# Optimization experiments

Hardware: AMD Instinct MI355X
Metric: run time of the kernel (lower is better)

The kernel has to match this reference:

```python
import jax, jax.numpy as jnp
import numpy as np

IMG_X, IMG_Y = 1333.0, 402.0   # image_size
MIN_SIZE = 16.0
NMS_THRESH = 0.7
PRE = 12000                    # n_train_pre_nms
POST = 2000                    # n_train_post_nms
HH, WW, A = 83, 25, 9          # 1333//16, 402//16, anchors per cell
N_ANCH = HH * WW * A           # 18675
B = 16


def setup_inputs() -> dict:
    key = jax.random.key(0)
    k1, k2, k3, k4, k5, k6 = jax.random.split(key, 6)
    # realistic anchor boxes inside the image
    xc = jax.random.uniform(k1, (N_ANCH,)) * IMG_X
    yc = jax.random.uniform(k2, (N_ANCH,)) * IMG_Y
    bw = jax.random.uniform(k3, (N_ANCH,)) * 240.0 + 16.0
    bh = jax.random.uniform(k4, (N_ANCH,)) * 120.0 + 16.0
    anchor_boxes = jnp.stack([xc - 0.5 * bw, yc - 0.5 * bh, xc + 0.5 * bw, yc + 0.5 * bh], axis=1)
    rpn_cls_score = jax.random.normal(k5, (B, N_ANCH * 2), dtype=jnp.float32)
    rpn_bbox_pred = jax.random.normal(k6, (B, N_ANCH, 4), dtype=jnp.float32) * 0.2
    return dict(anchor_boxes=anchor_boxes, rpn_cls_score=rpn_cls_score,
                rpn_bbox_pred=rpn_bbox_pred, rpn_cls_loss=jnp.zeros((1,), jnp.float32),
                rpn_bbox_loss=jnp.zeros((1,), jnp.float32))


def _decode(anchor_boxes, rpn_bbox_pred):
    ah = anchor_boxes[:, 3] - anchor_boxes[:, 1]
    aw = anchor_boxes[:, 2] - anchor_boxes[:, 0]
    acy = anchor_boxes[:, 1] + 0.5 * ah
    acx = anchor_boxes[:, 0] + 0.5 * aw
    dx = rpn_bbox_pred[..., 0]
    dy = rpn_bbox_pred[..., 1]
    dw = rpn_bbox_pred[..., 2]
    dh = rpn_bbox_pred[..., 3]
    cy = dy * ah + acy
    cx = dx * aw + acx
    h = jnp.exp(dh) * ah
    w = jnp.exp(dw) * aw
    # clip: x coords to [0, image_size[0]], y coords to [0, image_size[1]] (as in source)
    x1 = jnp.clip(cx - 0.5 * w, 0.0, IMG_X)
    y1 = jnp.clip(cy - 0.5 * h, 0.0, IMG_Y)
    x2 = jnp.clip(cx + 0.5 * w, 0.0, IMG_X)
    y2 = jnp.clip(cy + 0.5 * h, 0.0, IMG_Y)
    return jnp.stack([x1, y1, x2, y2], axis=-1)  # [N,4] broadcast over batch -> [B,N,4]


def _nms_one(roi, score):
    # roi: [N,4], score: [N]
    hs = roi[:, 3] - roi[:, 1]
    ws = roi[:, 2] - roi[:, 0]
    valid = (hs >= MIN_SIZE) & (ws >= MIN_SIZE)
    s = jnp.where(valid, score, -jnp.inf)
    idx = jnp.argsort(-s)[:PRE]          # score-descending, top pre_nms; invalid sink to end
    boxes = roi[idx]                      # score-sorted candidate boxes [PRE,4]
    vp = valid[idx]                       # which slots are real (passed size filter)
    # source quirk: order = order.argsort()[::-1] -> NMS visits boxes by DESCENDING
    # original-anchor-index; invalid slots get key -1 so they come last.
    seq_key = jnp.where(vp, idx, -1)
    perm = jnp.argsort(-seq_key)          # positions into score-sorted arrays, visit order
    x1, y1, x2, y2 = boxes[:, 0], boxes[:, 1], boxes[:, 2], boxes[:, 3]
    areas = (x2 - x1 + 1.0) * (y2 - y1 + 1.0)

    def step(alive, _):
        a_seq = alive[perm]
        any_alive = a_seq.any()
        j = perm[jnp.argmax(a_seq)]       # first surviving box in visit order
        xx1 = jnp.maximum(x1[j], x1)
        yy1 = jnp.maximum(y1[j], y1)
        xx2 = jnp.minimum(x2[j], x2)
        yy2 = jnp.minimum(y2[j], y2)
        inter = jnp.maximum(0.0, xx2 - xx1 + 1.0) * jnp.maximum(0.0, yy2 - yy1 + 1.0)
        ovr = inter / (areas[j] + areas - inter)
        alive = alive & jnp.where(any_alive, ovr <= NMS_THRESH, True)  # j kills itself (ovr=1)
        return alive, jnp.where(any_alive, j, -1)

    _, keep = jax.lax.scan(step, vp, None, length=POST)   # up to post_nms kept positions
    kmask = keep >= 0
    out = jnp.where(kmask[:, None], boxes[jnp.maximum(keep, 0)], 0.0)  # padded [POST,4]
    return out, kmask


def reference(anchor_boxes, rpn_cls_score, rpn_bbox_pred, rpn_cls_loss, rpn_bbox_loss):
    bsz = rpn_cls_score.shape[0]
    # objectness = view(B, 83, 25, 9, 2)[..., 1]
    score = rpn_cls_score.reshape(bsz, HH, WW, A, 2)[..., 1].reshape(bsz, -1)
    roi = _decode(anchor_boxes, rpn_bbox_pred)            # [B,N,4]
    rois, mask = jax.vmap(_nms_one)(roi, score)           # [B,POST,4], [B,POST]
    return rois, mask
```

## Files before the change

kernel.cpp:

```cpp
#include <hip/hip_runtime.h>
#include <math.h>

#define N_ANCHN 18675
#define NPAD    18688
#define BATCH   16
#define PRE     12000
#define CPAD    12032
#define WPB     188
#define POST    2000
#define NMS_T   0.7f
#define IMGX    1333.0f
#define IMGY    402.0f
#define MINSZ   16.0f
#define NBUCK   256
#define KINV    0x007FFFFFu
#define MLCAP   12288

typedef unsigned long long u64;

__device__ __forceinline__ unsigned key_of(float f) {
  unsigned u = __float_as_uint(f);
  return (u & 0x80000000u) ? ~u : (u | 0x80000000u);
}

__device__ __forceinline__ float iou_ref(float ax1, float ay1, float ax2, float ay2, float aar,
                                         float bx1, float by1, float bx2, float by2, float bar) {
  float xx1 = fmaxf(ax1, bx1);
  float yy1 = fmaxf(ay1, by1);
  float xx2 = fminf(ax2, bx2);
  float yy2 = fminf(ay2, by2);
  float iw = fmaxf(0.0f, __fadd_rn(__fsub_rn(xx2, xx1), 1.0f));
  float ih = fmaxf(0.0f, __fadd_rn(__fsub_rn(yy2, yy1), 1.0f));
  float inter = __fmul_rn(iw, ih);
  return __fdiv_rn(inter, __fsub_rn(__fadd_rn(aar, bar), inter));
}

__device__ __forceinline__ bool hit_test(float ix1, float iy1, float ix2, float iy2, float iar,
                                         float jx1, float jy1, float jx2, float jy2, float jar) {
  float xx1 = fmaxf(ix1, jx1);
  float yy1 = fmaxf(iy1, jy1);
  float xx2 = fminf(ix2, jx2);
  float yy2 = fminf(iy2, jy2);
  float iw = fmaxf(0.0f, __fadd_rn(__fsub_rn(xx2, xx1), 1.0f));
  float ih = fmaxf(0.0f, __fadd_rn(__fsub_rn(yy2, yy1), 1.0f));
  float inter = __fmul_rn(iw, ih);
  float S = __fadd_rn(iar, jar);
  if (inter >= __fmul_rn(0.43f, S)) return true;
  if (inter <= __fmul_rn(0.395f, S)) return false;
  return __fdiv_rn(inter, __fsub_rn(S, inter)) > NMS_T;
}

__device__ __forceinline__ void emit_hit(int lo, int hi, u64* diagb, unsigned* rcb,
                                         unsigned short* rtb, int L) {
  if ((hi >> 6) == (lo >> 6)) {
    atomicOr(&diagb[(size_t)(lo >> 6) * 64 + (hi & 63)], 1ull << (lo & 63));
  } else {
    unsigned slot = atomicAdd(&rcb[lo], 1u);
    if ((int)slot < L) rtb[(size_t)lo * L + slot] = (unsigned short)hi;
  }
}

__device__ __forceinline__ void decode_one(
    const float* __restrict__ anchors, const float* __restrict__ cls,
    const float* __restrict__ bbox, int b, int i,
    float& x1, float& y1, float& x2, float& y2, unsigned& key) {
  float4 A = *(const float4*)(anchors + (size_t)i * 4);
  float ah = __fsub_rn(A.w, A.y);
  float aw = __fsub_rn(A.z, A.x);
  float acy = __fadd_rn(A.y, __fmul_rn(0.5f, ah));
  float acx = __fadd_rn(A.x, __fmul_rn(0.5f, aw));

  float4 P = *(const float4*)(bbox + ((size_t)b * N_ANCHN + i) * 4);
  float dx = P.x, dy = P.y, dw = P.z, dh = P.w;

  float cy = __fadd_rn(__fmul_rn(dy, ah), acy);
  float cx = __fadd_rn(__fmul_rn(dx, aw), acx);
  float eh = (float)exp((double)dh);
  float ew = (float)exp((double)dw);
  float h = __fmul_rn(eh, ah);
  float w = __fmul_rn(ew, aw);

  x1 = fminf(fmaxf(__fsub_rn(cx, __fmul_rn(0.5f, w)), 0.0f), IMGX);
  y1 = fminf(fmaxf(__fsub_rn(cy, __fmul_rn(0.5f, h)), 0.0f), IMGY);
  x2 = fminf(fmaxf(__fadd_rn(cx, __fmul_rn(0.5f, w)), 0.0f), IMGX);
  y2 = fminf(fmaxf(__fadd_rn(cy, __fmul_rn(0.5f, h)), 0.0f), IMGY);

  bool valid = (__fsub_rn(y2, y1) >= MINSZ) && (__fsub_rn(x2, x1) >= MINSZ);
  float s = valid ? cls[(size_t)b * (2 * N_ANCHN) + 2 * i + 1] : -INFINITY;
  key = key_of(s);
}

__global__ __launch_bounds__(256) void decode_kernel(
    const float* __restrict__ anchors, const float* __restrict__ cls,
    const float* __restrict__ bbox,
    float* __restrict__ bx1, float* __restrict__ by1,
    float* __restrict__ bx2, float* __restrict__ by2,
    unsigned* __restrict__ keys,
    u64* __restrict__ diag, unsigned* __restrict__ rowcnt) {
  const int bx = blockIdx.x;
  const int b = blockIdx.y;
  if (bx == gridDim.x - 1) {
    u64* dz = diag + (size_t)b * WPB * 64;
    for (int i = threadIdx.x; i < WPB * 64; i += 256) dz[i] = 0ull;
    unsigned* rz = rowcnt + (size_t)b * CPAD;
    for (int i = threadIdx.x; i < CPAD; i += 256) rz[i] = 0u;
    return;
  }
  int i = bx * 256 + threadIdx.x;
  if (i >= N_ANCHN) return;
  float x1, y1, x2, y2; unsigned k;
  decode_one(anchors, cls, bbox, b, i, x1, y1, x2, y2, k);
  size_t o = (size_t)b * NPAD + i;
  bx1[o] = x1; by1[o] = y1; bx2[o] = x2; by2[o] = y2;
  keys[o] = k;
}

__global__ __launch_bounds__(1024) void prepsort_kernel(
    const unsigned* __restrict__ keys,
    const float* __restrict__ bx1, const float* __restrict__ by1,
    const float* __restrict__ bx2, const float* __restrict__ by2,
    float* __restrict__ cx1, float* __restrict__ cy1,
    float* __restrict__ cx2, float* __restrict__ cy2,
    float* __restrict__ car, int* __restrict__ ncand,
    float* __restrict__ sx1, float* __restrict__ sy1,
    float* __restrict__ sx2, float* __restrict__ sy2,
    float* __restrict__ sar, int* __restrict__ sperm,
    float* __restrict__ wminx1, float* __restrict__ wmaxx2) {
  const int b = blockIdx.x;
  const int tid = threadIdx.x;
  const int lane = tid & 63;
  const int wv = tid >> 6;
  __shared__ unsigned hist[16][256];
  __shared__ unsigned mh[256];
  __shared__ unsigned wsum[16];
  __shared__ unsigned bh[NBUCK];
  __shared__ unsigned boff[NBUCK];
  __shared__ unsigned char fb[NPAD];
  __shared__ unsigned short mlist[MLCAP];
  __shared__ unsigned sh_prefix, sh_k, sh_n, sh_mcount;
  const unsigned* kb = keys + (size_t)b * NPAD;

  if (tid == 0) { sh_prefix = 0u; sh_k = PRE; sh_mcount = 0u; }
  __syncthreads();

  {
    for (int idx = tid; idx < 16 * 256; idx += 1024) ((unsigned*)hist)[idx] = 0u;
    __syncthreads();
    for (int i = tid; i < N_ANCHN; i += 1024)
      atomicAdd(&hist[wv][kb[i] >> 24], 1u);
    __syncthreads();
    if (tid < 256) {
      unsigned s = 0;
#pragma unroll
      for (int q = 0; q < 16; ++q) s += hist[q][tid];
      mh[tid] = s;
    }
    __syncthreads();
    if (tid == 0) {
      unsigned kk = sh_k, cum = 0;
      for (int d = 255; d >= 0; --d) {
        unsigned c = mh[d];
        if (cum + c >= kk) { sh_k = kk - cum; sh_prefix = (unsigned)d << 24; break; }
        cum += c;
      }
    }
    __syncthreads();
  }

  {
    unsigned b0 = sh_prefix >> 24;
    for (int i = tid; i < N_ANCHN; i += 1024) {
      if ((kb[i] >> 24) == b0) {
        unsigned p = atomicAdd(&sh_mcount, 1u);
        if (p < MLCAP) mlist[p] = (unsigned short)i;
      }
    }
  }
  __syncthreads();
  const bool useList = (sh_mcount <= (unsigned)MLCAP);
  const unsigned mcount = min(sh_mcount, (unsigned)MLCAP);

  for (int level = 1; level < 4; ++level) {
    const int shift = 24 - 8 * level;
    for (int idx = tid; idx < 16 * 256; idx += 1024) ((unsigned*)hist)[idx] = 0u;
    __syncthreads();
    unsigned pre = sh_prefix;
    if (useList) {
      for (int idx = tid; idx < (int)mcount; idx += 1024) {
        unsigned k = kb[mlist[idx]];
        if ((k >> (shift + 8)) == (pre >> (shift + 8)))
          atomicAdd(&hist[wv][(k >> shift) & 255u], 1u);
      }
    } else {
      for (int i = tid; i < N_ANCHN; i += 1024) {
        unsigned k = kb[i];
        if ((k >> (shift + 8)) == (pre >> (shift + 8)))
          atomicAdd(&hist[wv][(k >> shift) & 255u], 1u);
      }
    }
    __syncthreads();
    if (tid < 256) {
      unsigned s = 0;
#pragma unroll
      for (int q = 0; q < 16; ++q) s += hist[q][tid];
      mh[tid] = s;
    }
    __syncthreads();
    if (tid == 0) {
      unsigned kk = sh_k, cum = 0;
      for (int d = 255; d >= 0; --d) {
        unsigned c = mh[d];
        if (cum + c >= kk) { sh_k = kk - cum; sh_prefix = pre | ((unsigned)d << shift); break; }
        cum += c;
      }
    }
    __syncthreads();
  }
  const unsigned T = sh_prefix;
  const unsigned slots = sh_k;

  const int SEG = (N_ANCHN + 1023) / 1024;

  {
    int i0 = tid * SEG, i1 = min(N_ANCHN, i0 + SEG);
    unsigned cnt = 0;
    for (int i = i0; i < i1; ++i) cnt += (kb[i] == T) ? 1u : 0u;
    unsigned v = cnt;
#pragma unroll
    for (int d = 1; d < 64; d <<= 1) {
      unsigned y = __shfl_up(v, d, 64);
      if (lane >= d) v += y;
    }
    if (lane == 63) wsum[wv] = v;
    __syncthreads();
    if (tid == 0) {
      unsigned acc = 0;
#pragma unroll
      for (int q = 0; q < 16; ++q) { unsigned t = wsum[q]; wsum[q] = acc; acc += t; }
    }
    __syncthreads();
    unsigned r = wsum[wv] + v - cnt;
    for (int i = i0; i < i1; ++i) {
      unsigned k = kb[i];
      bool tie = (k == T);
      bool cand = (k > T) || (tie && T > KINV && r < slots);
      if (tie) r++;
      fb[i] = cand ? (unsigned char)1 : (unsigned char)0;
    }
  }
  __syncthreads();

  const float* X1 = bx1 + (size_t)b * NPAD;
  const float* Y1 = by1 + (size_t)b * NPAD;
  const float* X2 = bx2 + (size_t)b * NPAD;
  const float* Y2 = by2 + (size_t)b * NPAD;
  {
    int j0 = tid * SEG, j1 = min(N_ANCHN, j0 + SEG);
    unsigned cnt = 0;
    for (int j = j0; j < j1; ++j) cnt += fb[N_ANCHN - 1 - j];
    unsigned v = cnt;
#pragma unroll
    for (int d = 1; d < 64; d <<= 1) {
      unsigned y = __shfl_up(v, d, 64);
      if (lane >= d) v += y;
    }
    if (lane == 63) wsum[wv] = v;
    __syncthreads();
    if (tid == 0) {
      unsigned acc = 0;
#pragma unroll
      for (int q = 0; q < 16; ++q) { unsigned t = wsum[q]; wsum[q] = acc; acc += t; }
      sh_n = acc;
    }
    __syncthreads();
    unsigned p = wsum[wv] + v - cnt;
    if (tid == 0) ncand[b] = (int)sh_n;
    float* CX1 = cx1 + (size_t)b * CPAD;
    float* CY1 = cy1 + (size_t)b * CPAD;
    float* CX2 = cx2 + (size_t)b * CPAD;
    float* CY2 = cy2 + (size_t)b * CPAD;
    float* CAR = car + (size_t)b * CPAD;
    for (int j = j0; j < j1; ++j) {
      int i = N_ANCHN - 1 - j;
      if (fb[i]) {
        float x1v = X1[i], y1v = Y1[i], x2v = X2[i], y2v = Y2[i];
        CX1[p] = x1v; CY1[p] = y1v; CX2[p] = x2v; CY2[p] = y2v;
        CAR[p] = __fmul_rn(__fadd_rn(__fsub_rn(x2v, x1v), 1.0f),
                           __fadd_rn(__fsub_rn(y2v, y1v), 1.0f));
        p++;
      }
    }
  }
  __syncthreads();
  const int n = (int)sh_n;

  const float scale = (float)NBUCK / 1334.0f;
  const float* CX1 = cx1 + (size_t)b * CPAD;
  const float* CY1 = cy1 + (size_t)b * CPAD;
  const float* CX2 = cx2 + (size_t)b * CPAD;
  const float* CY2 = cy2 + (size_t)b * CPAD;
  const float* CAR = car + (size_t)b * CPAD;
  float* SX1 = sx1 + (size_t)b * CPAD;
  float* SY1 = sy1 + (size_t)b * CPAD;
  float* SX2 = sx2 + (size_t)b * CPAD;
  float* SY2 = sy2 + (size_t)b * CPAD;
  float* SAR = sar + (size_t)b * CPAD;
  int* SP = sperm + (size_t)b * CPAD;

  if (tid < NBUCK) bh[tid] = 0u;
  __syncthreads();
  for (int i = tid; i < n; i += 1024) {
    int q = (int)(CX1[i] * scale);
    q = q < 0 ? 0 : (q > NBUCK - 1 ? NBUCK - 1 : q);
    atomicAdd(&bh[q], 1u);
  }
  __syncthreads();
  if (tid < 64) {
    unsigned carry = 0;
    for (int c = 0; c < 4; ++c) {
      unsigned own = bh[c * 64 + tid];
      unsigned v = own;
      for (int d = 1; d < 64; d <<= 1) {
        unsigned y = __shfl_up(v, d, 64);
        if (tid >= d) v += y;
      }
      boff[c * 64 + tid] = carry + v - own;
      carry += __shfl(v, 63, 64);
    }
  }
  __syncthreads();
  for (int i = tid; i < n; i += 1024) {
    float x1v = CX1[i];
    int q = (int)(x1v * scale);
    q = q < 0 ? 0 : (q > NBUCK - 1 ? NBUCK - 1 : q);
    unsigned p = atomicAdd(&boff[q], 1u);
    SX1[p] = x1v; SY1[p] = CY1[i]; SX2[p] = CX2[i]; SY2[p] = CY2[i];
    SAR[p] = CAR[i]; SP[p] = i;
  }
  for (int i = n + tid; i < CPAD; i += 1024) {
    SX1[i] = 1e30f; SY1[i] = 1e30f; SX2[i] = -1e30f; SY2[i] = -1e30f;
    SAR[i] = 1.0f; SP[i] = 0;
  }
  __syncthreads();
  for (int w = wv; w < WPB; w += 16) {
    float mn = SX1[64 * w + lane];
    float mx = SX2[64 * w + lane];
#pragma unroll
    for (int d = 32; d > 0; d >>= 1) {
      mn = fminf(mn, __shfl_xor(mn, d, 64));
      mx = fmaxf(mx, __shfl_xor(mx, d, 64));
    }
    if (lane == 0) {
      wminx1[(size_t)b * WPB + w] = mn;
      wmaxx2[(size_t)b * WPB + w] = mx;
    }
  }
}

__global__ __launch_bounds__(64) void build_kernel(
    const float* __restrict__ sx1, const float* __restrict__ sy1,
    const float* __restrict__ sx2, const float* __restrict__ sy2,
    const float* __restrict__ sar, const int* __restrict__ sperm,
    const int* __restrict__ ncand,
    const float* __restrict__ wminx1, const float* __restrict__ wmaxx2,
    u64* __restrict__ diagT, unsigned* __restrict__ rowcnt,
    unsigned short* __restrict__ rows_t, int L) {
  const int R = blockIdx.x, G = blockIdx.y, b = blockIdx.z;
  const int n = ncand[b];
  if (64 * R >= n) return;
  if (4 * G + 3 < R) return;
  const float* WMN = wminx1 + (size_t)b * WPB;
  const float rlim = __fadd_rn(wmaxx2[(size_t)b * WPB + R], 2.0f);

  const int w0 = 4 * G;
  const float wmn0 = WMN[w0], wmn1 = WMN[w0 + 1], wmn2 = WMN[w0 + 2], wmn3 = WMN[w0 + 3];
  const bool v0 = (w0     >= R) && (wmn0 <= rlim);
  const bool v1 = (w0 + 1 >= R) && (wmn1 <= rlim);
  const bool v2 = (w0 + 2 >= R) && (wmn2 <= rlim);
  const bool v3 = (w0 + 3 >= R) && (wmn3 <= rlim);
  if (!(v0 | v1 | v2 | v3)) return;

  const float* SX1 = sx1 + (size_t)b * CPAD;
  const float* SY1 = sy1 + (size_t)b * CPAD;
  const float* SX2 = sx2 + (size_t)b * CPAD;
  const float* SY2 = sy2 + (size_t)b * CPAD;
  const float* SAR = sar + (size_t)b * CPAD;
  const int* SP = sperm + (size_t)b * CPAD;

  const int lane = threadIdx.x;

  __shared__ float4 rbv[64];
  __shared__ float2 ras[64];
  float rx2own;
  {
    int i = 64 * R + lane;
    float4 v = make_float4(SX1[i], SY1[i], SX2[i], SY2[i]);
    rbv[lane] = v;
    ras[lane] = make_float2(SAR[i], __int_as_float(SP[i]));
    rx2own = v.z;
  }

  float c0x1 = 1e30f, c0y1 = 0.f, c0x2 = 0.f, c0y2 = 0.f, c0ar = 1.f; int c0sp = 0;
  float c1x1 = 1e30f, c1y1 = 0.f, c1x2 = 0.f, c1y2 = 0.f, c1ar = 1.f; int c1sp = 0;
  float c2x1 = 1e30f, c2y1 = 0.f, c2x2 = 0.f, c2y2 = 0.f, c2ar = 1.f; int c2sp = 0;
  float c3x1 = 1e30f, c3y1 = 0.f, c3x2 = 0.f, c3y2 = 0.f, c3ar = 1.f; int c3sp = 0;
  if (v0) { int j = 64 * w0 + lane;
    c0x1 = SX1[j]; c0y1 = SY1[j]; c0x2 = SX2[j]; c0y2 = SY2[j]; c0ar = SAR[j]; c0sp = SP[j]; }
  if (v1) { int j = 64 * (w0 + 1) + lane;
    c1x1 = SX1[j]; c1y1 = SY1[j]; c1x2 = SX2[j]; c1y2 = SY2[j]; c1ar = SAR[j]; c1sp = SP[j]; }
  if (v2) { int j = 64 * (w0 + 2) + lane;
    c2x1 = SX1[j]; c2y1 = SY1[j]; c2x2 = SX2[j]; c2y2 = SY2[j]; c2ar = SAR[j]; c2sp = SP[j]; }
  if (v3) { int j = 64 * (w0 + 3) + lane;
    c3x1 = SX1[j]; c3y1 = SY1[j]; c3x2 = SX2[j]; c3y2 = SY2[j]; c3ar = SAR[j]; c3sp = SP[j]; }
  __syncthreads();

  const float wmnlo = v0 ? wmn0 : (v1 ? wmn1 : (v2 ? wmn2 : wmn3));
  u64 a = __ballot(rx2own >= __fsub_rn(wmnlo, 2.0f));
  if (!a) return;

  const float wmn0m2 = __fsub_rn(wmn0, 2.0f);
  const float wmn1m2 = __fsub_rn(wmn1, 2.0f);
  const float wmn2m2 = __fsub_rn(wmn2, 2.0f);
  const float wmn3m2 = __fsub_rn(wmn3, 2.0f);
  const bool g0 = (w0 > R),     e0 = (w0 == R);
  const bool g1 = (w0 + 1 > R), e1 = (w0 + 1 == R);
  const bool g2 = (w0 + 2 > R), e2 = (w0 + 2 == R);
  const bool g3 = (w0 + 3 > R), e3 = (w0 + 3 == R);

  u64* diagb = diagT + (size_t)b * WPB * 64;
  unsigned* rcb = rowcnt + (size_t)b * CPAD;
  unsigned short* rtb = rows_t + (size_t)b * L * CPAD;

  int k = (int)__builtin_ctzll(a);
  float4 RB = rbv[k];
  float2 AS = ras[k];
  while (true) {
    a &= a - 1;
    const int kn = a ? (int)__builtin_ctzll(a) : 0;
    const float4 RBn = rbv[kn];
    const float2 ASn = ras[kn];
    const float rx2k = RB.z;
    const float rark = AS.x;
    const int rsp = __float_as_int(AS.y);
    if (v0 && rx2k >= wmn0m2) {
      bool dd = g0 | (e0 & (lane > k));
      if (dd && hit_test(RB.x, RB.y, RB.z, RB.w, rark, c0x1, c0y1, c0x2, c0y2, c0ar)) {
        int lo = min(rsp, c0sp), hi = max(rsp, c0sp);
        emit_hit(lo, hi, diagb, rcb, rtb, L);
      }
    }
    if (v1 && rx2k >= wmn1m2) {
      bool dd = g1 | (e1 & (lane > k));
      if (dd && hit_test(RB.x, RB.y, RB.z, RB.w, rark, c1x1, c1y1, c1x2, c1y2, c1ar)) {
        int lo = min(rsp, c1sp), hi = max(rsp, c1sp);
        emit_hit(lo, hi, diagb, rcb, rtb, L);
      }
    }
    if (v2 && rx2k >= wmn2m2) {
      bool dd = g2 | (e2 & (lane > k));
      if (dd && hit_test(RB.x, RB.y, RB.z, RB.w, rark, c2x1, c2y1, c2x2, c2y2, c2ar)) {
        int lo = min(rsp, c2sp), hi = max(rsp, c2sp);
        emit_hit(lo, hi, diagb, rcb, rtb, L);
      }
    }
    if (v3 && rx2k >= wmn3m2) {
      bool dd = g3 | (e3 & (lane > k));
      if (dd && hit_test(RB.x, RB.y, RB.z, RB.w, rark, c3x1, c3y1, c3x2, c3y2, c3ar)) {
        int lo = min(rsp, c3sp), hi = max(rsp, c3sp);
        emit_hit(lo, hi, diagb, rcb, rtb, L);
      }
    }
    if (!a) break;
    k = kn; RB = RBn; AS = ASn;
  }
}

#define DECLW(s) u64 kw##s; unsigned cw##s; uint4 p0##s, p1##s;
#define LOADW(s, wexp) { int w_ = (wexp); int c_ = 64 * w_ + lane; \
  kw##s = diagb[(size_t)w_ * 64 + lane]; cw##s = rcb[c_]; \
  const uint4* rp_ = (const uint4*)(rtb + (size_t)c_ * L); p0##s = rp_[0]; p1##s = rp_[1]; }
#define PROCW(s, wexp) { int w_ = (wexp); \
  if (w_ < nw && sc < POST) { \
    const int base_ = 64 * w_; const int myc_ = base_ + lane; \
    bool al = (myc_ < n) && !((supp[2 * w_ + (lane >> 5)] >> (lane & 31)) & 1u); \
    u64 act = __ballot(al); bool selme = false; \
    while (act && sc < POST) { \
      int j = (int)__builtin_ctzll(act); \
      if (lane == 0) sel[sc] = base_ + j; \
      sc++; selme |= (lane == j); \
      if ((kw##s >> j) & 1ull) al = false; \
      u64 gt = (j < 63) ? (~0ull << (j + 1)) : 0ull; \
      act = __ballot(al) & gt; } \
    if (selme) { \
      const int ce_ = min((int)cw##s, L); \
      uint4 p2_ = {0,0,0,0}, p3_ = {0,0,0,0}; \
      if (ce_ > 16) { \
        const uint4* rp_ = (const uint4*)(rtb + (size_t)myc_ * L); \
        p2_ = rp_[2]; p3_ = rp_[3]; \
      } \
      unsigned ev_[8] = {p0##s.x, p0##s.y, p0##s.z, p0##s.w, p1##s.x, p1##s.y, p1##s.z, p1##s.w}; \
      _Pragma("unroll") \
      for (int u_ = 0; u_ < 8; ++u_) { \
        if (2 * u_ < ce_)     { int t_ = (int)(ev_[u_] & 0xffffu); atomicOr(&supp[t_ >> 5], 1u << (t_ & 31)); } \
        if (2 * u_ + 1 < ce_) { int t_ = (int)(ev_[u_] >> 16);     atomicOr(&supp[t_ >> 5], 1u << (t_ & 31)); } } \
      if (ce_ > 16) { \
        unsigned e2_[8] = {p2_.x, p2_.y, p2_.z, p2_.w, p3_.x, p3_.y, p3_.z, p3_.w}; \
        _Pragma("unroll") \
        for (int u_ = 0; u_ < 8; ++u_) { \
          if (16 + 2 * u_ < ce_)     { int t_ = (int)(e2_[u_] & 0xffffu); atomicOr(&supp[t_ >> 5], 1u << (t_ & 31)); } \
          if (16 + 2 * u_ + 1 < ce_) { int t_ = (int)(e2_[u_] >> 16);     atomicOr(&supp[t_ >> 5], 1u << (t_ & 31)); } } } } \
    u64 om_ = __ballot(selme && ((int)cw##s > L)); \
    while (om_) { \
      int j_ = (int)__builtin_ctzll(om_); om_ &= om_ - 1; \
      const int mc_ = base_ + j_; \
      float ax1_ = CX1[mc_], ay1_ = CY1[mc_], ax2_ = CX2[mc_], ay2_ = CY2[mc_], aar_ = CAR[mc_]; \
      for (int c2_ = base_ + 64 + lane; c2_ < n; c2_ += 64) { \
        float ovr_ = iou_ref(ax1_, ay1_, ax2_, ay2_, aar_, CX1[c2_], CY1[c2_], CX2[c2_], CY2[c2_], CAR[c2_]); \
        if (ovr_ > NMS_T) atomicOr(&supp[c2_ >> 5], 1u << (c2_ & 31)); } } } }

__global__ __launch_bounds__(64) void scan_kernel(
    const float* __restrict__ cx1, const float* __restrict__ cy1,
    const float* __restrict__ cx2, const float* __restrict__ cy2,
    const float* __restrict__ car, const int* __restrict__ ncand,
    const u64* __restrict__ diagT, const unsigned* __restrict__ rowcnt,
    const unsigned short* __restrict__ rows_t, int L,
    float* __restrict__ out) {
  const int b = blockIdx.x;
  const int lane = threadIdx.x;
  __shared__ unsigned supp[2 * WPB];
  __shared__ int sel[POST];
  for (int idx = lane; idx < 2 * WPB; idx += 64) supp[idx] = 0u;

  const int n = ncand[b];
  const u64* diagb = diagT + (size_t)b * WPB * 64;
  const unsigned* rcb = rowcnt + (size_t)b * CPAD;
  const unsigned short* rtb = rows_t + (size_t)b * L * CPAD;
  const float* CX1 = cx1 + (size_t)b * CPAD;
  const float* CY1 = cy1 + (size_t)b * CPAD;
  const float* CX2 = cx2 + (size_t)b * CPAD;
  const float* CY2 = cy2 + (size_t)b * CPAD;
  const float* CAR = car + (size_t)b * CPAD;

  const int nw = (n + 63) >> 6;
  int sc = 0;

  DECLW(a0) DECLW(a1) DECLW(a2) DECLW(a3)
  DECLW(b0) DECLW(b1) DECLW(b2) DECLW(b3)

  if (nw > 0) {
    LOADW(a0, 0)
    LOADW(a1, min(1, WPB - 1))
    LOADW(a2, min(2, WPB - 1))
    LOADW(a3, min(3, WPB - 1))
    const int ng = (nw + 3) >> 2;
    for (int g = 0; g < ng && sc < POST; ++g) {
      const int wn = 4 * g + 4;
      LOADW(b0, min(wn + 0, WPB - 1))
      LOADW(b1, min(wn + 1, WPB - 1))
      LOADW(b2, min(wn + 2, WPB - 1))
      LOADW(b3, min(wn + 3, WPB - 1))
      PROCW(a0, 4 * g + 0)
      PROCW(a1, 4 * g + 1)
      PROCW(a2, 4 * g + 2)
      PROCW(a3, 4 * g + 3)
      kwa0 = kwb0; cwa0 = cwb0; p0a0 = p0b0; p1a0 = p1b0;
      kwa1 = kwb1; cwa1 = cwb1; p0a1 = p0b1; p1a1 = p1b1;
      kwa2 = kwb2; cwa2 = cwb2; p0a2 = p0b2; p1a2 = p1b2;
      kwa3 = kwb3; cwa3 = cwb3; p0a3 = p0b3; p1a3 = p1b3;
    }
  }

  float* roib = out + (size_t)b * POST * 4;
  float* maskb = out + (size_t)BATCH * POST * 4 + (size_t)b * POST;
  for (int t = lane; t < POST; t += 64) {
    if (t < sc) {
      int j = sel[t];
      float4 v = make_float4(CX1[j], CY1[j], CX2[j], CY2[j]);
      *(float4*)(roib + (size_t)t * 4) = v;
      maskb[t] = 1.0f;
    } else {
      *(float4*)(roib + (size_t)t * 4) = make_float4(0.f, 0.f, 0.f, 0.f);
      maskb[t] = 0.0f;
    }
  }
}

__global__ __launch_bounds__(256) void decode_fb_kernel(
    const float* __restrict__ anchors, const float* __restrict__ cls,
    const float* __restrict__ bbox,
    float* __restrict__ bx1, float* __restrict__ by1,
    float* __restrict__ bx2, float* __restrict__ by2,
    unsigned* __restrict__ keys) {
  int i = blockIdx.x * 256 + threadIdx.x;
  if (i >= N_ANCHN) return;
  int b = blockIdx.y;
  float x1, y1, x2, y2; unsigned k;
  decode_one(anchors, cls, bbox, b, i, x1, y1, x2, y2, k);
  size_t o = (size_t)b * NPAD + i;
  bx1[o] = x1; by1[o] = y1; bx2[o] = x2; by2[o] = y2;
  keys[o] = k;
}

__global__ __launch_bounds__(1024) void prep_kernel(
    const unsigned* __restrict__ keys,
    const float* __restrict__ bx1, const float* __restrict__ by1,
    const float* __restrict__ bx2, const float* __restrict__ by2,
    unsigned char* __restrict__ flags,
    float* __restrict__ cx1, float* __restrict__ cy1,
    float* __restrict__ cx2, float* __restrict__ cy2,
    float* __restrict__ car, int* __restrict__ ncand) {
  const int b = blockIdx.x;
  const int tid = threadIdx.x;
  __shared__ unsigned hist[256];
  __shared__ unsigned ssc[1024];
  __shared__ unsigned sh_prefix, sh_k;
  const unsigned* kb = keys + (size_t)b * NPAD;

  if (tid == 0) { sh_prefix = 0u; sh_k = PRE; }
  __syncthreads();

  for (int level = 0; level < 4; ++level) {
    const int shift = 24 - 8 * level;
    if (tid < 256) hist[tid] = 0u;
    __syncthreads();
    unsigned pre = sh_prefix;
    for (int i = tid; i < N_ANCHN; i += 1024) {
      unsigned k = kb[i];
      bool match = (level == 0) || ((k >> (shift + 8)) == (pre >> (shift + 8)));
      if (match) atomicAdd(&hist[(k >> shift) & 255u], 1u);
    }
    __syncthreads();
    if (tid == 0) {
      unsigned kk = sh_k, cum = 0;
      for (int d = 255; d >= 0; --d) {
        unsigned c = hist[d];
        if (cum + c >= kk) { sh_k = kk - cum; sh_prefix = pre | ((unsigned)d << shift); break; }
        cum += c;
      }
    }
    __syncthreads();
  }
  const unsigned T = sh_prefix;

  unsigned local = 0;
  for (int i = tid; i < N_ANCHN; i += 1024) local += (kb[i] > T) ? 1u : 0u;
  ssc[tid] = local;
  __syncthreads();
  for (int off = 512; off > 0; off >>= 1) {
    if (tid < off) ssc[tid] += ssc[tid + off];
    __syncthreads();
  }
  const unsigned slots = PRE - ssc[0];
  __syncthreads();

  const int SEG = (N_ANCHN + 1023) / 1024;
  const float* X1 = bx1 + (size_t)b * NPAD;
  const float* Y1 = by1 + (size_t)b * NPAD;
  const float* X2 = bx2 + (size_t)b * NPAD;
  const float* Y2 = by2 + (size_t)b * NPAD;
  unsigned char* fb = flags + (size_t)b * NPAD;

  {
    int i0 = tid * SEG, i1 = min(N_ANCHN, i0 + SEG);
    unsigned cnt = 0;
    for (int i = i0; i < i1; ++i) cnt += (kb[i] == T) ? 1u : 0u;
    ssc[tid] = cnt;
    __syncthreads();
    for (int off = 1; off < 1024; off <<= 1) {
      unsigned v = (tid >= off) ? ssc[tid - off] : 0u;
      __syncthreads();
      ssc[tid] += v;
      __syncthreads();
    }
    unsigned r = ssc[tid] - cnt;
    for (int i = i0; i < i1; ++i) {
      unsigned k = kb[i];
      bool valid = (__fsub_rn(Y2[i], Y1[i]) >= MINSZ) && (__fsub_rn(X2[i], X1[i]) >= MINSZ);
      bool tie = (k == T);
      bool cand = valid && ((k > T) || (tie && r < slots));
      if (tie) r++;
      fb[i] = cand ? (unsigned char)1 : (unsigned char)0;
    }
  }
  __syncthreads();

  {
    int j0 = tid * SEG, j1 = min(N_ANCHN, j0 + SEG);
    unsigned cnt = 0;
    for (int j = j0; j < j1; ++j) cnt += fb[N_ANCHN - 1 - j];
    ssc[tid] = cnt;
    __syncthreads();
    for (int off = 1; off < 1024; off <<= 1) {
      unsigned v = (tid >= off) ? ssc[tid - off] : 0u;
      __syncthreads();
      ssc[tid] += v;
      __syncthreads();
    }
    unsigned p = ssc[tid] - cnt;
    if (tid == 0) ncand[b] = (int)ssc[1023];
    float* CX1 = cx1 + (size_t)b * CPAD;
    float* CY1 = cy1 + (size_t)b * CPAD;
    float* CX2 = cx2 + (size_t)b * CPAD;
    float* CY2 = cy2 + (size_t)b * CPAD;
    float* CAR = car + (size_t)b * CPAD;
    for (int j = j0; j < j1; ++j) {
      int i = N_ANCHN - 1 - j;
      if (fb[i]) {
        float x1v = X1[i], y1v = Y1[i], x2v = X2[i], y2v = Y2[i];
        CX1[p] = x1v; CY1[p] = y1v; CX2[p] = x2v; CY2[p] = y2v;
        CAR[p] = __fmul_rn(__fadd_rn(__fsub_rn(x2v, x1v), 1.0f),
                           __fadd_rn(__fsub_rn(y2v, y1v), 1.0f));
        p++;
      }
    }
  }
}

__global__ __launch_bounds__(1024) void nms_kernel(
    const float* __restrict__ cx1, const float* __restrict__ cy1,
    const float* __restrict__ cx2, const float* __restrict__ cy2,
    const float* __restrict__ car, const int* __restrict__ ncand,
    float* __restrict__ out) {
  const int b = blockIdx.x;
  const int tid = threadIdx.x;
  __shared__ float sx1[POST], sy1[POST], sx2[POST], sy2[POST], sar[POST];
  __shared__ int Lbuf[1024];
  __shared__ int wcount[16];
  __shared__ int sh_sc;

  const float* CX1 = cx1 + (size_t)b * CPAD;
  const float* CY1 = cy1 + (size_t)b * CPAD;
  const float* CX2 = cx2 + (size_t)b * CPAD;
  const float* CY2 = cy2 + (size_t)b * CPAD;
  const float* CAR = car + (size_t)b * CPAD;
  float* roib = out + (size_t)b * POST * 4;
  float* maskb = out + (size_t)BATCH * POST * 4 + (size_t)b * POST;

  const int n = ncand[b];
  if (tid == 0) sh_sc = 0;
  __syncthreads();
  const int lane = tid & 63;
  const int w = tid >> 6;

  for (int base = 0; base < n; base += 1024) {
    const int c = base + tid;
    bool pass = (c < n);
    float px1 = 0, py1 = 0, px2 = 0, py2 = 0, par = 0;
    if (pass) { px1 = CX1[c]; py1 = CY1[c]; px2 = CX2[c]; py2 = CY2[c]; par = CAR[c]; }
    const int sc0 = sh_sc;

    if (pass) {
      for (int k = 0; k < sc0; ++k) {
        float ovr = iou_ref(sx1[k], sy1[k], sx2[k], sy2[k], sar[k], px1, py1, px2, py2, par);
        if (ovr > NMS_T) { pass = false; break; }
      }
    }

    unsigned long long bal = __ballot(pass);
    if (lane == 0) wcount[w] = (int)__popcll(bal);
    __syncthreads();
    int off = 0;
    for (int q = 0; q < 16; ++q) off += (q < w) ? wcount[q] : 0;
    if (pass) Lbuf[off + (int)__popcll(bal & ((1ULL << lane) - 1ULL))] = c;
    __syncthreads();

    if (tid < 64) {
      int total = 0;
      for (int q = 0; q < 16; ++q) total += wcount[q];
      int sc = sc0;
      for (int g = 0; g < total && sc < POST; g += 64) {
        int idx = (g + lane < total) ? Lbuf[g + lane] : -1;
        float qx1 = 0, qy1 = 0, qx2 = 0, qy2 = 0, qar = 0;
        bool al = (idx >= 0);
        if (al) { qx1 = CX1[idx]; qy1 = CY1[idx]; qx2 = CX2[idx]; qy2 = CY2[idx]; qar = CAR[idx]; }
        for (int k = sc0; k < sc && al; ++k) {
          float ovr = iou_ref(sx1[k], sy1[k], sx2[k], sy2[k], sar[k], qx1, qy1, qx2, qy2, qar);
          if (ovr > NMS_T) al = false;
        }
        unsigned long long alive = __ballot(al);
        while (alive && sc < POST) {
          int j = (int)__builtin_ctzll(alive);
          float jx1 = __shfl(qx1, j), jy1 = __shfl(qy1, j);
          float jx2 = __shfl(qx2, j), jy2 = __shfl(qy2, j), jar = __shfl(qar, j);
          float ovr = iou_ref(jx1, jy1, jx2, jy2, jar, qx1, qy1, qx2, qy2, qar);
          unsigned long long killm = __ballot(ovr > NMS_T);
          alive &= ~killm;
          alive &= ~(1ULL << j);
          if (lane == 0) {
            sx1[sc] = jx1; sy1[sc] = jy1; sx2[sc] = jx2; sy2[sc] = jy2; sar[sc] = jar;
            roib[(size_t)sc * 4 + 0] = jx1;
            roib[(size_t)sc * 4 + 1] = jy1;
            roib[(size_t)sc * 4 + 2] = jx2;
            roib[(size_t)sc * 4 + 3] = jy2;
          }
          sc++;
        }
      }
      if (lane == 0) sh_sc = sc;
    }
    __syncthreads();
    if (sh_sc >= POST) break;
  }
  __syncthreads();

  const int sc = sh_sc;
  for (int t = tid; t < POST; t += 1024) {
    if (t >= sc) {
      roib[(size_t)t * 4 + 0] = 0.f; roib[(size_t)t * 4 + 1] = 0.f;
      roib[(size_t)t * 4 + 2] = 0.f; roib[(size_t)t * 4 + 3] = 0.f;
    }
    maskb[t] = (t < sc) ? 1.0f : 0.0f;
  }
}

extern "C" void kernel_launch(void* const* d_in, const int* in_sizes, int n_in,
                              void* d_out, int out_size, void* d_ws, size_t ws_size,
                              hipStream_t stream) {
  const float* anchors = (const float*)d_in[0];
  const float* cls = (const float*)d_in[1];
  const float* bbox = (const float*)d_in[2];
  float* out = (float*)d_out;
  char* ws = (char*)d_ws;

  size_t o = 0;
  float* cx1 = (float*)(ws + o); o += (size_t)BATCH * CPAD * 4;
  float* cy1 = (float*)(ws + o); o += (size_t)BATCH * CPAD * 4;
  float* cx2 = (float*)(ws + o); o += (size_t)BATCH * CPAD * 4;
  float* cy2 = (float*)(ws + o); o += (size_t)BATCH * CPAD * 4;
  float* car = (float*)(ws + o); o += (size_t)BATCH * CPAD * 4;
  int* ncand = (int*)(ws + o); o += 256;
  u64* diag = (u64*)(ws + o); o += (size_t)BATCH * WPB * 64 * 8;
  unsigned* rowcnt = (unsigned*)(ws + o); o += (size_t)BATCH * CPAD * 4;
  float* wminx1 = (float*)(ws + o); o += (size_t)BATCH * WPB * 4;
  float* wmaxx2 = (float*)(ws + o); o += (size_t)BATCH * WPB * 4;
  float* sx1 = (float*)(ws + o); o += (size_t)BATCH * CPAD * 4;
  float* sy1 = (float*)(ws + o); o += (size_t)BATCH * CPAD * 4;
  float* sx2 = (float*)(ws + o); o += (size_t)BATCH * CPAD * 4;
  float* sy2 = (float*)(ws + o); o += (size_t)BATCH * CPAD * 4;
  float* sar = (float*)(ws + o); o += (size_t)BATCH * CPAD * 4;
  int* sperm = (int*)(ws + o); o += (size_t)BATCH * CPAD * 4;
  size_t overlay = o;
  unsigned* keys = (unsigned*)(ws + overlay);
  float* bx1 = (float*)(ws + overlay + (size_t)BATCH * NPAD * 4 * 1);
  float* by1 = (float*)(ws + overlay + (size_t)BATCH * NPAD * 4 * 2);
  float* bx2 = (float*)(ws + overlay + (size_t)BATCH * NPAD * 4 * 3);
  float* by2 = (float*)(ws + overlay + (size_t)BATCH * NPAD * 4 * 4);
  size_t decode_bytes = (size_t)BATCH * NPAD * 4 * 5;
  unsigned short* rows_t = (unsigned short*)(ws + overlay);

  int L = 0;
  for (int Ltry = 32; Ltry >= 16; Ltry -= 16) {
    size_t rows_bytes = (size_t)BATCH * Ltry * CPAD * 2;
    size_t need = overlay + (decode_bytes > rows_bytes ? decode_bytes : rows_bytes);
    if (ws_size >= need) { L = Ltry; break; }
  }

  if (L > 0) {
    dim3 dgrid((N_ANCHN + 255) / 256 + 1, BATCH);
    decode_kernel<<<dgrid, 256, 0, stream>>>(anchors, cls, bbox, bx1, by1, bx2, by2,
                                             keys, diag, rowcnt);
    prepsort_kernel<<<BATCH, 1024, 0, stream>>>(keys, bx1, by1, bx2, by2,
                                                cx1, cy1, cx2, cy2, car, ncand,
                                                sx1, sy1, sx2, sy2, sar, sperm,
                                                wminx1, wmaxx2);
    build_kernel<<<dim3(WPB, (WPB + 3) / 4, BATCH), 64, 0, stream>>>(
        sx1, sy1, sx2, sy2, sar, sperm, ncand, wminx1, wmaxx2,
        diag, rowcnt, rows_t, L);
    scan_kernel<<<BATCH, 64, 0, stream>>>(cx1, cy1, cx2, cy2, car, ncand,
                                          diag, rowcnt, rows_t, L, out);
  } else {
    size_t f = 0;
    unsigned* fkeys = (unsigned*)(ws + f); f += (size_t)BATCH * NPAD * 4;
    float* fbx1 = (float*)(ws + f); f += (size_t)BATCH * NPAD * 4;
    float* fby1 = (float*)(ws + f); f += (size_t)BATCH * NPAD * 4;
    float* fbx2 = (float*)(ws + f); f += (size_t)BATCH * NPAD * 4;
    float* fby2 = (float*)(ws + f); f += (size_t)BATCH * NPAD * 4;
    float* fcx1 = (float*)(ws + f); f += (size_t)BATCH * CPAD * 4;
    float* fcy1 = (float*)(ws + f); f += (size_t)BATCH * CPAD * 4;
    float* fcx2 = (float*)(ws + f); f += (size_t)BATCH * CPAD * 4;
    float* fcy2 = (float*)(ws + f); f += (size_t)BATCH * CPAD * 4;
    float* fcar = (float*)(ws + f); f += (size_t)BATCH * CPAD * 4;
    unsigned char* fflags = (unsigned char*)(ws + f); f += (size_t)BATCH * NPAD;
    int* fncand = (int*)(ws + f); f += 256;

    dim3 dgrid((N_ANCHN + 255) / 256, BATCH);
    decode_fb_kernel<<<dgrid, 256, 0, stream>>>(anchors, cls, bbox, fbx1, fby1, fbx2, fby2, fkeys);
    prep_kernel<<<BATCH, 1024, 0, stream>>>(fkeys, fbx1, fby1, fbx2, fby2, fflags,
                                            fcx1, fcy1, fcx2, fcy2, fcar, fncand);
    nms_kernel<<<BATCH, 1024, 0, stream>>>(fcx1, fcy1, fcx2, fcy2, fcar, fncand, out);
  }
}
```

Baseline: 644.9 us.

## Transpose diagonal suppression masks and resolve intra-word NMS with readlane

The within-word diagonal mask is transposed so each lane holds the bitmask of later boxes it suppresses. The serial greedy selection then uses readlane plus mask clearing instead of a ballot per selected box, and selected indices are written to sel by popcount rank. The shared suppression bitmap moves from 32-bit to 64-bit words, so each 64-candidate group is read with one load and marked with 64-bit LDS atomics. The intent is to shorten the serial dependency chain in the scan kernel; the cost is 64-bit atomics and a readlane per selected box.

```diff
diff --git a/kernel.cpp b/kernel.cpp
--- a/kernel.cpp
+++ b/kernel.cpp
@@ -53,7 +53,7 @@
 __device__ __forceinline__ void emit_hit(int lo, int hi, u64* diagb, unsigned* rcb,
                                          unsigned short* rtb, int L) {
   if ((hi >> 6) == (lo >> 6)) {
-    atomicOr(&diagb[(size_t)(lo >> 6) * 64 + (hi & 63)], 1ull << (lo & 63));
+    atomicOr(&diagb[(size_t)(lo >> 6) * 64 + (lo & 63)], 1ull << (hi & 63));
   } else {
     unsigned slot = atomicAdd(&rcb[lo], 1u);
     if ((int)slot < L) rtb[(size_t)lo * L + slot] = (unsigned short)hi;
@@ -482,16 +482,22 @@
 #define PROCW(s, wexp) { int w_ = (wexp); \
   if (w_ < nw && sc < POST) { \
     const int base_ = 64 * w_; const int myc_ = base_ + lane; \
-    bool al = (myc_ < n) && !((supp[2 * w_ + (lane >> 5)] >> (lane & 31)) & 1u); \
-    u64 act = __ballot(al); bool selme = false; \
-    while (act && sc < POST) { \
-      int j = (int)__builtin_ctzll(act); \
-      if (lane == 0) sel[sc] = base_ + j; \
-      sc++; selme |= (lane == j); \
-      if ((kw##s >> j) & 1ull) al = false; \
-      u64 gt = (j < 63) ? (~0ull << (j + 1)) : 0ull; \
-      act = __ballot(al) & gt; } \
-    if (selme) { \
+    const u64 suppw_ = supp[w_]; \
+    const bool alv_ = (myc_ < n) && !((suppw_ >> lane) & 1ull); \
+    u64 act_ = __ballot(alv_); \
+    u64 selw_ = 0ull; \
+    const int scb_ = sc; \
+    const unsigned klo_ = (unsigned)kw##s, khi_ = (unsigned)(kw##s >> 32); \
+    while (act_ && sc < POST) { \
+      const int j_ = (int)__builtin_ctzll(act_); \
+      const u64 kj_ = ((u64)(unsigned)__builtin_amdgcn_readlane((int)khi_, j_) << 32) | \
+                      (u64)(unsigned)__builtin_amdgcn_readlane((int)klo_, j_); \
+      selw_ |= 1ull << j_; sc++; \
+      act_ &= ~(kj_ | (1ull << j_)); } \
+    const bool selme_ = ((selw_ >> lane) & 1ull) != 0ull; \
+    if (selme_) { \
+      const int rank_ = scb_ + (int)__popcll(selw_ & ((1ull << lane) - 1ull)); \
+      sel[rank_] = myc_; \
       const int ce_ = min((int)cw##s, L); \
       uint4 p2_ = {0,0,0,0}, p3_ = {0,0,0,0}; \
       if (ce_ > 16) { \
@@ -501,22 +507,22 @@
       unsigned ev_[8] = {p0##s.x, p0##s.y, p0##s.z, p0##s.w, p1##s.x, p1##s.y, p1##s.z, p1##s.w}; \
       _Pragma("unroll") \
       for (int u_ = 0; u_ < 8; ++u_) { \
-        if (2 * u_ < ce_)     { int t_ = (int)(ev_[u_] & 0xffffu); atomicOr(&supp[t_ >> 5], 1u << (t_ & 31)); } \
-        if (2 * u_ + 1 < ce_) { int t_ = (int)(ev_[u_] >> 16);     atomicOr(&supp[t_ >> 5], 1u << (t_ & 31)); } } \
+        if (2 * u_ < ce_)     { int t_ = (int)(ev_[u_] & 0xffffu); atomicOr(&supp[t_ >> 6], 1ull << (t_ & 63)); } \
+        if (2 * u_ + 1 < ce_) { int t_ = (int)(ev_[u_] >> 16);     atomicOr(&supp[t_ >> 6], 1ull << (t_ & 63)); } } \
       if (ce_ > 16) { \
         unsigned e2_[8] = {p2_.x, p2_.y, p2_.z, p2_.w, p3_.x, p3_.y, p3_.z, p3_.w}; \
         _Pragma("unroll") \
         for (int u_ = 0; u_ < 8; ++u_) { \
-          if (16 + 2 * u_ < ce_)     { int t_ = (int)(e2_[u_] & 0xffffu); atomicOr(&supp[t_ >> 5], 1u << (t_ & 31)); } \
-          if (16 + 2 * u_ + 1 < ce_) { int t_ = (int)(e2_[u_] >> 16);     atomicOr(&supp[t_ >> 5], 1u << (t_ & 31)); } } } } \
-    u64 om_ = __ballot(selme && ((int)cw##s > L)); \
+          if (16 + 2 * u_ < ce_)     { int t_ = (int)(e2_[u_] & 0xffffu); atomicOr(&supp[t_ >> 6], 1ull << (t_ & 63)); } \
+          if (16 + 2 * u_ + 1 < ce_) { int t_ = (int)(e2_[u_] >> 16);     atomicOr(&supp[t_ >> 6], 1ull << (t_ & 63)); } } } } \
+    u64 om_ = __ballot(selme_ && ((int)cw##s > L)); \
     while (om_) { \
       int j_ = (int)__builtin_ctzll(om_); om_ &= om_ - 1; \
       const int mc_ = base_ + j_; \
       float ax1_ = CX1[mc_], ay1_ = CY1[mc_], ax2_ = CX2[mc_], ay2_ = CY2[mc_], aar_ = CAR[mc_]; \
       for (int c2_ = base_ + 64 + lane; c2_ < n; c2_ += 64) { \
         float ovr_ = iou_ref(ax1_, ay1_, ax2_, ay2_, aar_, CX1[c2_], CY1[c2_], CX2[c2_], CY2[c2_], CAR[c2_]); \
-        if (ovr_ > NMS_T) atomicOr(&supp[c2_ >> 5], 1u << (c2_ & 31)); } } } }
+        if (ovr_ > NMS_T) atomicOr(&supp[c2_ >> 6], 1ull << (c2_ & 63)); } } } }
 
 __global__ __launch_bounds__(64) void scan_kernel(
     const float* __restrict__ cx1, const float* __restrict__ cy1,
@@ -527,9 +533,9 @@
     float* __restrict__ out) {
   const int b = blockIdx.x;
   const int lane = threadIdx.x;
-  __shared__ unsigned supp[2 * WPB];
+  __shared__ u64 supp[WPB];
   __shared__ int sel[POST];
-  for (int idx = lane; idx < 2 * WPB; idx += 64) supp[idx] = 0u;
+  for (int idx = lane; idx < WPB; idx += 64) supp[idx] = 0ull;
 
   const int n = ncand[b];
   const u64* diagb = diagT + (size_t)b * WPB * 64;
```

New measurement: 543.5 us. -15.7%, faster.
